# Kernel tuning notes

Measured on AMD Instinct MI355X. Metric: run time of the kernel, lower is better.

## Reference

```python
import jax, jax.numpy as jnp
import numpy as np

B, T, D = 4, 1024, 2048
H = 32
HD = D // H  # 64
NEG = -1e9


def setup_inputs() -> dict:
    key = jax.random.key(0)
    ks = jax.random.split(key, 12)
    s = 0.02
    x = jax.random.normal(ks[0], (B, T, D), dtype=jnp.float32)
    # additive causal mask [1, 1, T, T]
    causal = jnp.tril(jnp.ones((T, T), dtype=bool))
    attention_mask = jnp.where(causal, 0.0, NEG).astype(jnp.float32)[None, None]
    cache = jnp.zeros((B, 2, T, H, HD), dtype=jnp.float32)
    return {
        "x": x,
        "attention_mask": attention_mask,
        "cache": cache,
        "cache_update_index": 0,
        "Wq": jax.random.normal(ks[1], (D, D), jnp.float32) * s,
        "bq": jnp.zeros((D,), jnp.float32),
        "Wk": jax.random.normal(ks[2], (D, D), jnp.float32) * s,
        "bk": jnp.zeros((D,), jnp.float32),
        "Wv": jax.random.normal(ks[3], (D, D), jnp.float32) * s,
        "bv": jnp.zeros((D,), jnp.float32),
        "Wo": jax.random.normal(ks[4], (D, D), jnp.float32) * s,
        "bo": jnp.zeros((D,), jnp.float32),
    }


def _split_heads(t):
    b, s, _ = t.shape
    return t.reshape(b, s, H, HD).transpose(0, 2, 1, 3)  # (B,H,T,HD)


def reference(x, attention_mask, cache, cache_update_index, Wq, bq, Wk, bk, Wv, bv, Wo, bo):
    q = _split_heads(x @ Wq + bq)  # (B,H,T,HD)
    k = _split_heads(x @ Wk + bk)
    v = _split_heads(x @ Wv + bv)

    # update KV cache (cache layout: [B, 2, max_len, H, HD])
    k_for_cache = k.transpose(0, 2, 1, 3)  # (B,T,H,HD)
    v_for_cache = v.transpose(0, 2, 1, 3)
    idx = (0, cache_update_index, 0, 0)
    k_cache = jax.lax.dynamic_update_slice(cache[:, 0], k_for_cache, idx)
    v_cache = jax.lax.dynamic_update_slice(cache[:, 1], v_for_cache, idx)
    new_cache = jnp.stack([k_cache, v_cache], axis=1)
    k = k_cache.transpose(0, 2, 1, 3)  # (B,H,S,HD)
    v = v_cache.transpose(0, 2, 1, 3)

    scale = jnp.asarray(HD, q.dtype) ** -0.5
    scores = jnp.einsum("bhqd,bhkd->bhqk", q, k) * scale + attention_mask.astype(q.dtype)
    attn = jax.nn.softmax(scores, axis=-1)
    ctx = jnp.einsum("bhqk,bhkd->bhqd", attn, v)  # (B,H,T,HD)
    merged = ctx.transpose(0, 2, 1, 3).reshape(x.shape[0], x.shape[1], D)
    out = merged @ Wo + bo
    return out, new_cache
```

## Files before the change

### kernel.cpp

```cpp
#include <hip/hip_runtime.h>
#include <hip/hip_bf16.h>
#include <stdint.h>


typedef __hip_bfloat16 bf16;
typedef unsigned short us;
typedef short s16x8 __attribute__((ext_vector_type(8)));
typedef float f32x4 __attribute__((ext_vector_type(4)));

#define T_SEQ   1024
#define D_MODEL 2048

__device__ inline us f2b(float f) {
    bf16 h = __float2bfloat16(f);
    return *(us*)&h;
}

typedef __attribute__((address_space(1))) const void gas_void;
typedef __attribute__((address_space(3))) void las_void;

__device__ inline void gl2lds16(const void* g, void* l) {
    __builtin_amdgcn_global_load_lds((gas_void*)g, (las_void*)l, 16, 0, 0);
}

__global__ __launch_bounds__(256)
void cvtx_kernel(const float* __restrict__ x, us* __restrict__ xb)
{
    const size_t i = ((size_t)blockIdx.x * 256 + threadIdx.x) * 8;
    float4 a = *(const float4*)(x + i);
    float4 b = *(const float4*)(x + i + 4);
    union { uint4 u; us s[8]; } p;
    p.s[0] = f2b(a.x); p.s[1] = f2b(a.y); p.s[2] = f2b(a.z); p.s[3] = f2b(a.w);
    p.s[4] = f2b(b.x); p.s[5] = f2b(b.y); p.s[6] = f2b(b.z); p.s[7] = f2b(b.w);
    *(uint4*)(xb + i) = p.u;
}

__global__ __launch_bounds__(256)
void wtrans_kernel(const float* __restrict__ W0, const float* __restrict__ W1,
                   us* __restrict__ Wt)
{
    __shared__ float tile[64][65];
    const int z = blockIdx.z;
    const float* W = (z == 0) ? W0 : W1;
    us* dst = Wt + (size_t)z * D_MODEL * D_MODEL;

    const int tid = threadIdx.x;
    const int k0 = blockIdx.y * 64, n0 = blockIdx.x * 64;

    const int rr = tid >> 4, cc = (tid & 15) * 4;
    #pragma unroll
    for (int i = 0; i < 4; ++i) {
        float4 v = *(const float4*)(W + (size_t)(k0 + rr + i * 16) * D_MODEL + n0 + cc);
        tile[rr + i * 16][cc]     = v.x;
        tile[rr + i * 16][cc + 1] = v.y;
        tile[rr + i * 16][cc + 2] = v.z;
        tile[rr + i * 16][cc + 3] = v.w;
    }
    __syncthreads();

    const int nr = tid >> 3, kc = (tid & 7) * 8;
    #pragma unroll
    for (int i = 0; i < 2; ++i) {
        const int n = nr + i * 32;
        union { uint4 u; us s[8]; } p;
        #pragma unroll
        for (int j = 0; j < 8; ++j) p.s[j] = f2b(tile[kc + j][n]);
        *(uint4*)(dst + (size_t)(n0 + n) * D_MODEL + k0 + kc) = p.u;
    }
}

template<int MODE>
__global__ __launch_bounds__(256, 3)
void gemm128_kernel(const us* __restrict__ A, const us* __restrict__ Bt,
                    const float* __restrict__ b0, const float* __restrict__ b1,
                    float* __restrict__ out0, float* __restrict__ out1,
                    us* __restrict__ vbt, const int* __restrict__ idxp)
{
    __shared__ __align__(16) us As[128 * 64];
    __shared__ __align__(16) us Bs[128 * 64];

    const int tid  = threadIdx.x;
    const int wv   = tid >> 6;
    const int lane = tid & 63;
    const int quad = lane >> 4;
    const int l15  = lane & 15;
    const int wm   = wv >> 1;
    const int wn   = wv & 1;

    const int gx  = gridDim.x;
    const int nwg = gx * gridDim.y;
    int bid = blockIdx.y * gx + blockIdx.x;
    bid = (bid & 7) * (nwg >> 3) + (bid >> 3);
    const int m0 = (bid / gx) * 128;
    const int n0 = (bid % gx) * 128;

    const int srow = lane >> 3;
    const int scol = ((lane & 7) ^ srow) * 8;
    const us* aG = A  + (size_t)(m0 + wv * 32 + srow) * D_MODEL + scol;
    const us* bG = Bt + (size_t)(n0 + wv * 32 + srow) * D_MODEL + scol;
    us* aL = As + wv * 32 * 64;
    us* bL = Bs + wv * 32 * 64;

    f32x4 acc[4][4];
    #pragma unroll
    for (int mi = 0; mi < 4; ++mi)
        #pragma unroll
        for (int ni = 0; ni < 4; ++ni) acc[mi][ni] = f32x4{0.f, 0.f, 0.f, 0.f};

    const int xr = l15 & 7;
    #define LDA(MI, KK) (*(const s16x8*)(As + (wm * 64 + (MI) * 16 + l15) * 64 \
                          + ((((KK) * 4 + quad) ^ xr) * 8)))
    #define LDB(NI, KK) (*(const s16x8*)(Bs + (wn * 64 + (NI) * 16 + l15) * 64 \
                          + ((((KK) * 4 + quad) ^ xr) * 8)))

    for (int k0 = 0; k0 < D_MODEL; k0 += 64) {
        #pragma unroll
        for (int g = 0; g < 4; ++g) {
            gl2lds16(aG + k0 + g * 8 * D_MODEL, aL + g * 512);
            gl2lds16(bG + k0 + g * 8 * D_MODEL, bL + g * 512);
        }
        __syncthreads();

        #pragma unroll
        for (int kk = 0; kk < 2; ++kk) {
            s16x8 af[4], bfr[4];
            #pragma unroll
            for (int mi = 0; mi < 4; ++mi) af[mi] = LDA(mi, kk);
            #pragma unroll
            for (int ni = 0; ni < 4; ++ni) bfr[ni] = LDB(ni, kk);
            #pragma unroll
            for (int mi = 0; mi < 4; ++mi)
                #pragma unroll
                for (int ni = 0; ni < 4; ++ni)
                    acc[mi][ni] = __builtin_amdgcn_mfma_f32_16x16x32_bf16(
                        af[mi], bfr[ni], acc[mi][ni], 0, 0, 0);
        }
        __syncthreads();
    }
    #undef LDA
    #undef LDB

    const int seg = (MODE == 4) ? (n0 >> 11) : 0;
    const float* bias = (MODE == 4) ? (seg == 0 ? b0 : b1) : b0;
    const int idx = (MODE == 0) ? 0 : idxp[0];

    #pragma unroll
    for (int ni = 0; ni < 4; ++ni) {
        const int col = n0 + wn * 64 + ni * 16 + l15;
        const int cl  = col & (D_MODEL - 1);
        const float bv = bias[cl];
        #pragma unroll
        for (int mi = 0; mi < 4; ++mi) {
            float vv[4];
            #pragma unroll
            for (int r = 0; r < 4; ++r) {
                const int m = m0 + wm * 64 + mi * 16 + quad * 4 + r;
                const float v = acc[mi][ni][r] + bv;
                if (MODE == 0) {
                    out0[(size_t)m * D_MODEL + cl] = v;
                } else if (MODE == 4) {
                    if (seg == 0) {
                        ((us*)out0)[(size_t)m * D_MODEL + cl] = f2b(v * 0.125f);
                    } else {
                        const int b  = m >> 10;
                        const int tt = ((m & 1023) + idx) & 1023;
                        out1[((size_t)(b * 2 + 0) * T_SEQ + tt) * D_MODEL + cl] = v;
                    }
                } else {
                    const int b  = m >> 10;
                    const int tt = ((m & 1023) + idx) & 1023;
                    out1[((size_t)(b * 2 + 1) * T_SEQ + tt) * D_MODEL + cl] = v;
                    vv[r] = v;
                }
            }
            if (MODE == 5) {
                const int tok0 = m0 + wm * 64 + mi * 16 + quad * 4;
                const int bb = tok0 >> 10, t0 = tok0 & 1023;
                const int hh = cl >> 6, dd = cl & 63;
                ushort4 pv;
                pv.x = f2b(vv[0]); pv.y = f2b(vv[1]);
                pv.z = f2b(vv[2]); pv.w = f2b(vv[3]);
                *(ushort4*)(vbt + (size_t)((bb * 32 + hh) * 64 + dd) * 1024 + t0) = pv;
            }
        }
    }
}

#define LDW 72

__global__ __launch_bounds__(512, 4)
void attn_mfma_kernel(const us* __restrict__ q, const float* __restrict__ cache,
                      const us* __restrict__ vbt, us* __restrict__ ctx)
{
    __shared__ __align__(16) us Qs[128 * LDW];
    __shared__ __align__(16) us Ks[2][64 * LDW];
    __shared__ __align__(16) us Vt[2][64 * 64];

    const int tid  = threadIdx.x;
    const int wave = tid >> 6;
    const int lane = tid & 63;
    const int quad = lane >> 4;
    const int l15  = lane & 15;
    const int xr   = l15 & 7;

    const int bh = blockIdx.x;
    const int b  = bh >> 5;
    const int h  = bh & 31;
    const int qt = 7 - blockIdx.y;

    const float* kbase = cache + ((size_t)(b * 2 + 0) * T_SEQ) * D_MODEL + h * 64;
    const us* vb_bh = vbt + (size_t)((b * 32 + h) * 64) * 1024;

    {
        const int qrow = tid >> 2;
        const int qp   = tid & 3;
        const uint4* qg = (const uint4*)(q + (size_t)(b * T_SEQ + qt * 128 + qrow) * D_MODEL
                                           + h * 64 + qp * 16);
        uint4 q0 = qg[0], q1 = qg[1];
        *(uint4*)(Qs + qrow * LDW + qp * 16)     = q0;
        *(uint4*)(Qs + qrow * LDW + qp * 16 + 8) = q1;
    }

    const int ksrow = tid >> 3;
    const int kp8   = tid & 7;
    const int vrow  = lane >> 3;
    const int vchk  = (lane & 7) ^ vrow;
    const us* vG = vb_bh + (size_t)(wave * 8 + vrow) * 1024 + vchk * 8;

    const int nkt = 2 * qt + 2;

    gl2lds16(vG, (us*)Vt[0] + wave * 512);
    {
        const float4* kg = (const float4*)(kbase + (size_t)ksrow * D_MODEL + kp8 * 8);
        float4 k0 = kg[0], k1 = kg[1];
        union { uint4 u; us s[8]; } p;
        p.s[0] = f2b(k0.x); p.s[1] = f2b(k0.y); p.s[2] = f2b(k0.z); p.s[3] = f2b(k0.w);
        p.s[4] = f2b(k1.x); p.s[5] = f2b(k1.y); p.s[6] = f2b(k1.z); p.s[7] = f2b(k1.w);
        *(uint4*)(&Ks[0][ksrow * LDW + kp8 * 8]) = p.u;
    }
    __syncthreads();

    const s16x8 qf0 = *(const s16x8*)(Qs + (wave * 16 + l15) * LDW + quad * 8);
    const s16x8 qf1 = *(const s16x8*)(Qs + (wave * 16 + l15) * LDW + 32 + quad * 8);

    f32x4 oacc[4];
    #pragma unroll
    for (int t = 0; t < 4; ++t) oacc[t] = f32x4{0.f, 0.f, 0.f, 0.f};
    float m_run[4] = {-1e30f, -1e30f, -1e30f, -1e30f};
    float l_run[4] = {0.f, 0.f, 0.f, 0.f};

    for (int kt = 0; kt < nkt; ++kt) {
        const int buf = kt & 1;
        const bool more = (kt + 1 < nkt);

        float4 nk0, nk1;
        if (more) {
            gl2lds16(vG + (kt + 1) * 64, (us*)Vt[buf ^ 1] + wave * 512);
            const float4* kg = (const float4*)(kbase
                + (size_t)((kt + 1) * 64 + ksrow) * D_MODEL + kp8 * 8);
            nk0 = kg[0]; nk1 = kg[1];
        }

        const int kbr = kt * 64 - qt * 128;
        if (kbr < wave * 16 + 16) {
            const us* kb_ = Ks[buf];
            const us* vb_ = (const us*)Vt[buf];

            f32x4 sacc[4];
            #pragma unroll
            for (int t = 0; t < 4; ++t) sacc[t] = f32x4{0.f, 0.f, 0.f, 0.f};
            #pragma unroll
            for (int t = 0; t < 4; ++t) {
                s16x8 kf0 = *(const s16x8*)(kb_ + (t * 16 + l15) * LDW + quad * 8);
                s16x8 kf1 = *(const s16x8*)(kb_ + (t * 16 + l15) * LDW + 32 + quad * 8);
                sacc[t] = __builtin_amdgcn_mfma_f32_16x16x32_bf16(qf0, kf0, sacc[t], 0, 0, 0);
                sacc[t] = __builtin_amdgcn_mfma_f32_16x16x32_bf16(qf1, kf1, sacc[t], 0, 0, 0);
            }

            if (kbr + 63 > wave * 16) {
                #pragma unroll
                for (int t = 0; t < 4; ++t) {
                    const int keyl = kbr + t * 16 + l15;
                    #pragma unroll
                    for (int r = 0; r < 4; ++r) {
                        if (keyl > wave * 16 + quad * 4 + r) sacc[t][r] = -1e30f;
                    }
                }
            }

            float rmax[4];
            #pragma unroll
            for (int r = 0; r < 4; ++r)
                rmax[r] = fmaxf(fmaxf(sacc[0][r], sacc[1][r]), fmaxf(sacc[2][r], sacc[3][r]));
            #pragma unroll
            for (int off = 1; off < 16; off <<= 1) {
                #pragma unroll
                for (int r = 0; r < 4; ++r) rmax[r] = fmaxf(rmax[r], __shfl_xor(rmax[r], off, 16));
            }
            float alpha[4];
            #pragma unroll
            for (int r = 0; r < 4; ++r) {
                const float mnew = fmaxf(m_run[r], rmax[r]);
                alpha[r] = __expf(m_run[r] - mnew);
                m_run[r] = mnew;
            }
            float rsum[4] = {0.f, 0.f, 0.f, 0.f};
            #pragma unroll
            for (int t = 0; t < 4; ++t) {
                #pragma unroll
                for (int r = 0; r < 4; ++r) {
                    const float p = __expf(sacc[t][r] - m_run[r]);
                    sacc[t][r] = p;
                    rsum[r] += p;
                }
            }
            #pragma unroll
            for (int off = 1; off < 16; off <<= 1) {
                #pragma unroll
                for (int r = 0; r < 4; ++r) rsum[r] += __shfl_xor(rsum[r], off, 16);
            }
            #pragma unroll
            for (int r = 0; r < 4; ++r) l_run[r] = l_run[r] * alpha[r] + rsum[r];
            #pragma unroll
            for (int t = 0; t < 4; ++t) {
                #pragma unroll
                for (int r = 0; r < 4; ++r) oacc[t][r] *= alpha[r];
            }

            #pragma unroll
            for (int t = 0; t < 4; ++t) {
                #pragma unroll
                for (int r = 0; r < 4; ++r)
                    Qs[(wave * 16 + quad * 4 + r) * LDW + t * 16 + l15] = f2b(sacc[t][r]);
            }

            s16x8 pf0 = *(const s16x8*)(Qs + (wave * 16 + l15) * LDW + quad * 8);
            s16x8 pf1 = *(const s16x8*)(Qs + (wave * 16 + l15) * LDW + 32 + quad * 8);
            #pragma unroll
            for (int t = 0; t < 4; ++t) {
                s16x8 vf0 = *(const s16x8*)(vb_ + (t * 16 + l15) * 64 + ((quad ^ xr) * 8));
                s16x8 vf1 = *(const s16x8*)(vb_ + (t * 16 + l15) * 64 + (((4 + quad) ^ xr) * 8));
                oacc[t] = __builtin_amdgcn_mfma_f32_16x16x32_bf16(pf0, vf0, oacc[t], 0, 0, 0);
                oacc[t] = __builtin_amdgcn_mfma_f32_16x16x32_bf16(pf1, vf1, oacc[t], 0, 0, 0);
            }
        }

        if (more) {
            union { uint4 u; us s[8]; } p;
            p.s[0] = f2b(nk0.x); p.s[1] = f2b(nk0.y); p.s[2] = f2b(nk0.z); p.s[3] = f2b(nk0.w);
            p.s[4] = f2b(nk1.x); p.s[5] = f2b(nk1.y); p.s[6] = f2b(nk1.z); p.s[7] = f2b(nk1.w);
            *(uint4*)(&Ks[buf ^ 1][ksrow * LDW + kp8 * 8]) = p.u;
        }
        __syncthreads();
    }

    float invl[4];
    #pragma unroll
    for (int r = 0; r < 4; ++r) invl[r] = 1.0f / l_run[r];
    #pragma unroll
    for (int r = 0; r < 4; ++r) {
        const int qrow = qt * 128 + wave * 16 + quad * 4 + r;
        us* orow = ctx + (size_t)(b * T_SEQ + qrow) * D_MODEL + h * 64;
        #pragma unroll
        for (int t = 0; t < 4; ++t) orow[t * 16 + l15] = f2b(oacc[t][r] * invl[r]);
    }
}

extern "C" void kernel_launch(void* const* d_in, const int* in_sizes, int n_in,
                              void* d_out, int out_size, void* d_ws, size_t ws_size,
                              hipStream_t stream)
{
    const float* x    = (const float*)d_in[0];
    const int*   idxp = (const int*)d_in[3];
    const float* Wq   = (const float*)d_in[4];
    const float* bq   = (const float*)d_in[5];
    const float* Wk   = (const float*)d_in[6];
    const float* bk   = (const float*)d_in[7];
    const float* Wv   = (const float*)d_in[8];
    const float* bv   = (const float*)d_in[9];
    const float* Wo   = (const float*)d_in[10];
    const float* bo   = (const float*)d_in[11];

    float* out      = (float*)d_out;
    us*    xb       = (us*)d_out;
    us*    qb       = (us*)d_out + (size_t)8 * 1024 * 1024;
    float* cacheOut = out + (size_t)4 * T_SEQ * D_MODEL;

    us* WTqk = (us*)d_ws;
    us* WTv  = (us*)d_ws + (size_t)8 * 1024 * 1024;
    us* vbt  = (us*)d_ws;
    us* ctxb = (us*)d_ws + (size_t)8 * 1024 * 1024;
    us* WTo  = (us*)d_ws;

    const dim3 tb(256);

    cvtx_kernel<<<dim3(4096), tb, 0, stream>>>(x, xb);
    wtrans_kernel<<<dim3(32, 32, 2), tb, 0, stream>>>(Wq, Wk, WTqk);

    gemm128_kernel<4><<<dim3(32, 32), tb, 0, stream>>>(
        xb, WTqk, bq, bk, (float*)qb, cacheOut, nullptr, idxp);

    wtrans_kernel<<<dim3(32, 32, 1), tb, 0, stream>>>(Wv, Wv, WTv);

    gemm128_kernel<5><<<dim3(16, 32), tb, 0, stream>>>(
        xb, WTv, bv, nullptr, nullptr, cacheOut, vbt, idxp);

    attn_mfma_kernel<<<dim3(128, 8), dim3(512), 0, stream>>>(qb, cacheOut, vbt, ctxb);

    wtrans_kernel<<<dim3(32, 32, 1), tb, 0, stream>>>(Wo, Wo, WTo);

    gemm128_kernel<0><<<dim3(16, 32), tb, 0, stream>>>(
        ctxb, WTo, bo, nullptr, out, nullptr, nullptr, nullptr);
}
```

Measured before the change: 441.6 us.

## Merge Q, K and V projections into one GEMM and transpose V separately

After: 437.6 us. Within noise of the previous version (-0.9%).

```diff
diff --git a/kernel.cpp b/kernel.cpp
--- a/kernel.cpp
+++ b/kernel.cpp
@@ -37,11 +37,11 @@
 
 __global__ __launch_bounds__(256)
 void wtrans_kernel(const float* __restrict__ W0, const float* __restrict__ W1,
-                   us* __restrict__ Wt)
+                   const float* __restrict__ W2, us* __restrict__ Wt)
 {
     __shared__ float tile[64][65];
     const int z = blockIdx.z;
-    const float* W = (z == 0) ? W0 : W1;
+    const float* W = (z == 0) ? W0 : (z == 1) ? W1 : W2;
     us* dst = Wt + (size_t)z * D_MODEL * D_MODEL;
 
     const int tid = threadIdx.x;
@@ -69,12 +69,46 @@
     }
 }
 
+__global__ __launch_bounds__(256)
+void v2t_kernel(const float* __restrict__ cache, us* __restrict__ vbt)
+{
+    __shared__ float tile[64][65];
+    const int t0 = blockIdx.x * 64;
+    const int h  = blockIdx.y;
+    const int b  = blockIdx.z;
+
+    const float* src = cache + ((size_t)(b * 2 + 1) * T_SEQ) * D_MODEL + h * 64;
+
+    const int tid = threadIdx.x;
+    const int rr = tid >> 4, cc = (tid & 15) * 4;
+    #pragma unroll
+    for (int i = 0; i < 4; ++i) {
+        float4 v = *(const float4*)(src + (size_t)(t0 + rr + i * 16) * D_MODEL + cc);
+        tile[rr + i * 16][cc]     = v.x;
+        tile[rr + i * 16][cc + 1] = v.y;
+        tile[rr + i * 16][cc + 2] = v.z;
+        tile[rr + i * 16][cc + 3] = v.w;
+    }
+    __syncthreads();
+
+    const int dr = tid >> 3, tc = (tid & 7) * 8;
+    #pragma unroll
+    for (int i = 0; i < 2; ++i) {
+        const int d = dr + i * 32;
+        union { uint4 u; us s[8]; } p;
+        #pragma unroll
+        for (int j = 0; j < 8; ++j) p.s[j] = f2b(tile[tc + j][d]);
+        *(uint4*)(vbt + (size_t)((b * 32 + h) * 64 + d) * 1024 + t0 + tc) = p.u;
+    }
+}
+
 template<int MODE>
 __global__ __launch_bounds__(256, 3)
 void gemm128_kernel(const us* __restrict__ A, const us* __restrict__ Bt,
                     const float* __restrict__ b0, const float* __restrict__ b1,
+                    const float* __restrict__ b2,
                     float* __restrict__ out0, float* __restrict__ out1,
-                    us* __restrict__ vbt, const int* __restrict__ idxp)
+                    const int* __restrict__ idxp)
 {
     __shared__ __align__(16) us As[128 * 64];
     __shared__ __align__(16) us Bs[128 * 64];
@@ -140,9 +174,9 @@
     #undef LDA
     #undef LDB
 
-    const int seg = (MODE == 4) ? (n0 >> 11) : 0;
-    const float* bias = (MODE == 4) ? (seg == 0 ? b0 : b1) : b0;
-    const int idx = (MODE == 0) ? 0 : idxp[0];
+    const int seg = (MODE == 3) ? (n0 >> 11) : 0;
+    const float* bias = (MODE == 3) ? (seg == 0 ? b0 : (seg == 1 ? b1 : b2)) : b0;
+    const int idx = (MODE == 3 && seg > 0) ? idxp[0] : 0;
 
     #pragma unroll
     for (int ni = 0; ni < 4; ++ni) {
@@ -151,36 +185,21 @@
         const float bv = bias[cl];
         #pragma unroll
         for (int mi = 0; mi < 4; ++mi) {
-            float vv[4];
             #pragma unroll
             for (int r = 0; r < 4; ++r) {
                 const int m = m0 + wm * 64 + mi * 16 + quad * 4 + r;
                 const float v = acc[mi][ni][r] + bv;
                 if (MODE == 0) {
                     out0[(size_t)m * D_MODEL + cl] = v;
-                } else if (MODE == 4) {
+                } else {
                     if (seg == 0) {
                         ((us*)out0)[(size_t)m * D_MODEL + cl] = f2b(v * 0.125f);
                     } else {
                         const int b  = m >> 10;
                         const int tt = ((m & 1023) + idx) & 1023;
-                        out1[((size_t)(b * 2 + 0) * T_SEQ + tt) * D_MODEL + cl] = v;
+                        out1[((size_t)(b * 2 + (seg - 1)) * T_SEQ + tt) * D_MODEL + cl] = v;
                     }
-                } else {
-                    const int b  = m >> 10;
-                    const int tt = ((m & 1023) + idx) & 1023;
-                    out1[((size_t)(b * 2 + 1) * T_SEQ + tt) * D_MODEL + cl] = v;
-                    vv[r] = v;
                 }
-            }
-            if (MODE == 5) {
-                const int tok0 = m0 + wm * 64 + mi * 16 + quad * 4;
-                const int bb = tok0 >> 10, t0 = tok0 & 1023;
-                const int hh = cl >> 6, dd = cl & 63;
-                ushort4 pv;
-                pv.x = f2b(vv[0]); pv.y = f2b(vv[1]);
-                pv.z = f2b(vv[2]); pv.w = f2b(vv[3]);
-                *(ushort4*)(vbt + (size_t)((bb * 32 + hh) * 64 + dd) * 1024 + t0) = pv;
             }
         }
     }
@@ -386,8 +405,7 @@
     us*    qb       = (us*)d_out + (size_t)8 * 1024 * 1024;
     float* cacheOut = out + (size_t)4 * T_SEQ * D_MODEL;
 
-    us* WTqk = (us*)d_ws;
-    us* WTv  = (us*)d_ws + (size_t)8 * 1024 * 1024;
+    us* WT3  = (us*)d_ws;
     us* vbt  = (us*)d_ws;
     us* ctxb = (us*)d_ws + (size_t)8 * 1024 * 1024;
     us* WTo  = (us*)d_ws;
@@ -395,20 +413,17 @@
     const dim3 tb(256);
 
     cvtx_kernel<<<dim3(4096), tb, 0, stream>>>(x, xb);
-    wtrans_kernel<<<dim3(32, 32, 2), tb, 0, stream>>>(Wq, Wk, WTqk);
-
-    gemm128_kernel<4><<<dim3(32, 32), tb, 0, stream>>>(
-        xb, WTqk, bq, bk, (float*)qb, cacheOut, nullptr, idxp);
-
-    wtrans_kernel<<<dim3(32, 32, 1), tb, 0, stream>>>(Wv, Wv, WTv);
-
-    gemm128_kernel<5><<<dim3(16, 32), tb, 0, stream>>>(
-        xb, WTv, bv, nullptr, nullptr, cacheOut, vbt, idxp);
+    wtrans_kernel<<<dim3(32, 32, 3), tb, 0, stream>>>(Wq, Wk, Wv, WT3);
+
+    gemm128_kernel<3><<<dim3(48, 32), tb, 0, stream>>>(
+        xb, WT3, bq, bk, bv, (float*)qb, cacheOut, idxp);
+
+    v2t_kernel<<<dim3(16, 32, 4), tb, 0, stream>>>(cacheOut, vbt);
 
     attn_mfma_kernel<<<dim3(128, 8), dim3(512), 0, stream>>>(qb, cacheOut, vbt, ctxb);
 
-    wtrans_kernel<<<dim3(32, 32, 1), tb, 0, stream>>>(Wo, Wo, WTo);
+    wtrans_kernel<<<dim3(32, 32, 1), tb, 0, stream>>>(Wo, Wo, Wo, WTo);
 
     gemm128_kernel<0><<<dim3(16, 32), tb, 0, stream>>>(
-        ctxb, WTo, bo, nullptr, out, nullptr, nullptr, nullptr);
-}
+        ctxb, WTo, bo, nullptr, nullptr, out, nullptr, nullptr);
+}
```
